# Performance work log

Measured on AMD Instinct MI355X. Metric: run time of the kernel, lower is better.

Reference implementation:

```python
import jax, jax.numpy as jnp
import numpy as np

ATTN_SCALE = 0.12
HEAD_DIM = 128


def _rms_norm(x):
    # F.rms_norm with no weight; eps defaults to machine eps of dtype
    eps = jnp.asarray(jnp.finfo(x.dtype).eps, x.dtype)
    return x * jax.lax.rsqrt(jnp.mean(x * x, axis=-1, keepdims=True) + eps)


def _rope(x):
    # x: [B, T, H, D]; standard rotary over (first-half, second-half) pairs
    T, D = x.shape[1], x.shape[-1]
    half = D // 2
    inv_freq = 1.0 / (10000.0 ** (jnp.arange(half, dtype=jnp.float32) / half))
    ang = jnp.arange(T, dtype=jnp.float32)[:, None] * inv_freq[None, :]  # [T, half]
    cos = jnp.cos(ang)[None, :, None, :].astype(x.dtype)
    sin = jnp.sin(ang)[None, :, None, :].astype(x.dtype)
    x1, x2 = x[..., :half], x[..., half:]
    return jnp.concatenate([x1 * cos - x2 * sin, x1 * sin + x2 * cos], axis=-1)


def setup_inputs() -> dict:
    key = jax.random.key(0)
    ks = jax.random.split(key, 4)
    B, T, dim, H, hd = 4, 2048, 1024, 8, HEAD_DIM
    hdim = H * hd
    std = 0.5 * dim ** (-0.5)
    bound = (3.0 ** 0.5) * std
    return {
        "x": jax.random.normal(ks[0], (B, T, dim), jnp.float32),
        "ve": jax.random.normal(ks[1], (B, T, hdim), jnp.float32),
        "qkv_w": jax.random.uniform(ks[2], (3, hdim, dim), jnp.float32, -bound, bound),
        "lambdas": jnp.array([0.5, 0.5], jnp.float32),
        "c_proj_w": jax.random.normal(ks[3], (dim, hdim), jnp.float32) * (hdim ** -0.5),
        "c_proj_b": jnp.zeros((dim,), jnp.float32),
    }


def reference(x, ve, qkv_w, lambdas, c_proj_w, c_proj_b):
    B, T, dim = x.shape
    hdim = qkv_w.shape[1]
    hd = HEAD_DIM
    H = hdim // hd
    # fused QKV projection: [B,T,3,H,hd]
    qkv = jnp.einsum('btd,ehd->bteh', x, qkv_w.reshape(3 * hdim, dim).reshape(3 * H, hd, dim).reshape(3 * hdim // hd, hd, dim))
    qkv = jnp.einsum('btd,fd->btf', x, qkv_w.reshape(3 * hdim, dim)).reshape(B, T, 3, H, hd)
    q, k, v = qkv[:, :, 0], qkv[:, :, 1], qkv[:, :, 2]  # each [B,T,H,hd]
    q, k = _rms_norm(q), _rms_norm(k)
    q, k = _rope(q), _rope(k)
    v = lambdas[0] * v + lambdas[1] * ve.reshape(B, T, H, hd)
    # causal SDPA with custom scale
    scores = jnp.einsum('bthd,bshd->bhts', q, k) * ATTN_SCALE  # [B,H,T,T]
    causal = jnp.tril(jnp.ones((T, T), dtype=bool))
    scores = jnp.where(causal[None, None], scores, jnp.finfo(scores.dtype).min)
    p = jax.nn.softmax(scores, axis=-1)
    y = jnp.einsum('bhts,bshd->bthd', p, v).reshape(B, T, hdim)
    return y @ c_proj_w.T + c_proj_b
```

## Files before the change

### kernel.cpp

```cpp
#include <hip/hip_runtime.h>
#include <math.h>

typedef unsigned short u16;
typedef short bf16x8 __attribute__((ext_vector_type(8)));
typedef u16 u16x2 __attribute__((ext_vector_type(2)));
typedef u16 u16x4 __attribute__((ext_vector_type(4)));
typedef u16 u16x8 __attribute__((ext_vector_type(8)));
typedef float f32x2 __attribute__((ext_vector_type(2)));
typedef float f32x4 __attribute__((ext_vector_type(4)));
typedef float f32x16 __attribute__((ext_vector_type(16)));

typedef __attribute__((address_space(1))) const void gvoid_t;
typedef __attribute__((address_space(3))) void lvoid_t;

__device__ __forceinline__ u16 f2bf(float f) {
  union { float f; unsigned u; } v; v.f = f;
  unsigned r = v.u + 0x7fffu + ((v.u >> 16) & 1u);
  return (u16)(r >> 16);
}
__device__ __forceinline__ float bf2f(u16 h) {
  union { unsigned u; float f; } v; v.u = ((unsigned)h) << 16;
  return v.f;
}
__device__ __forceinline__ f32x4 mfma16(bf16x8 a, bf16x8 b, f32x4 c) {
  return __builtin_amdgcn_mfma_f32_16x16x32_bf16(a, b, c, 0, 0, 0);
}
__device__ __forceinline__ f32x16 mfma32(bf16x8 a, bf16x8 b, f32x16 c) {
  return __builtin_amdgcn_mfma_f32_32x32x16_bf16(a, b, c, 0, 0, 0);
}
__device__ __forceinline__ void gload_lds16(const void* g, void* l) {
  __builtin_amdgcn_global_load_lds((gvoid_t*)g, (lvoid_t*)l, 16, 0, 0);
}
__device__ __forceinline__ unsigned cvtpk_bf16(float lo, float hi) {
  unsigned r;
  asm("v_cvt_pk_bf16_f32 %0, %1, %2" : "=v"(r) : "v"(lo), "v"(hi));
  return r;
}
__device__ __forceinline__ void pswap32(unsigned& a, unsigned& b) {
  asm("v_permlane32_swap_b32 %0, %1" : "+v"(a), "+v"(b));
}

#if __has_builtin(__builtin_amdgcn_exp2f)
#define EXPW(x) __builtin_amdgcn_exp2f(x)
#define SCALE_W 0.17312354f
#define DEFER_THR 11.5415603f
#else
#define EXPW(x) __expf(x)
#define SCALE_W 0.12f
#define DEFER_THR 8.0f
#endif

#define BAR() __builtin_amdgcn_s_barrier()
#define WAITLGKM()                          \
  asm volatile("s_waitcnt lgkmcnt(0)");     \
  __builtin_amdgcn_sched_barrier(0)
#define WAITVMC(N)                                    \
  do {                                                \
    __builtin_amdgcn_s_waitcnt(0x0F70 | (N));         \
    __builtin_amdgcn_sched_barrier(0);                \
  } while (0)

__global__ __launch_bounds__(256) void cvt_bf16_kernel(const float* __restrict__ in,
                                                       u16* __restrict__ out, int n4) {
  int i = blockIdx.x * 256 + threadIdx.x;
  if (i >= n4) return;
  f32x4 v = *(const f32x4*)(in + (size_t)i * 4);
  u16x4 o;
  o[0] = f2bf(v[0]); o[1] = f2bf(v[1]); o[2] = f2bf(v[2]); o[3] = f2bf(v[3]);
  *(u16x4*)(out + (size_t)i * 4) = o;
}

__global__ __launch_bounds__(256) void rope_tab_kernel(float* __restrict__ ct,
                                                       float* __restrict__ st) {
  int i = blockIdx.x * 256 + threadIdx.x;
  int t = i >> 6, j = i & 63;
  float inv = powf(10000.f, -(float)j * (1.0f / 64.0f));
  float ang = (float)t * inv;
  ct[i] = cosf(ang);
  st[i] = sinf(ang);
}

template <int BM, int OUTF32>
__global__ __launch_bounds__(512, 1) void gemm8p_kernel(
    const u16* __restrict__ A, const u16* __restrict__ B, void* __restrict__ C,
    const float* __restrict__ bias, int M, int N, int K, int nbn) {
  constexpr int AH = BM / 2;
  constexpr int WR = AH / 2;
  constexpr int MI = WR / 16;
  constexpr int NACC = 2 * MI;
  constexpr int AROUNDS = AH / 64;
  constexpr int SA = AROUNDS;
  constexpr int SB = 2;
  __shared__ u16 Alds[2][BM * 64];
  __shared__ u16 Blds[2][256 * 64];
  int nwg = gridDim.x;
  int cpx = nwg >> 3;
  int bid = blockIdx.x;
  int swz = (bid & 7) * cpx + (bid >> 3);
  int bm = swz / nbn, bn = swz % nbn;
  size_t m0 = (size_t)bm * BM, n0 = (size_t)bn * 256;
  int tid = threadIdx.x, wid = tid >> 6, lane = tid & 63;
  int wr = wid >> 2, wc = wid & 3, l15 = lane & 15, l4 = lane >> 4;
  int srow = tid >> 3, sch = tid & 7;

  const u16* Abase = A + m0 * K;
  const u16* Bbase = B + n0 * K;

  f32x4 acc[NACC][4];
#pragma unroll
  for (int m = 0; m < NACC; m++)
#pragma unroll
    for (int n = 0; n < 4; n++) acc[m][n] = f32x4{0.f, 0.f, 0.f, 0.f};

  auto stageA = [&](int buf, int kt, int half) {
#pragma unroll
    for (int r = 0; r < AROUNDS; ++r) {
      int row = AH * half + 64 * r + srow;
      gload_lds16(Abase + (size_t)row * K + kt * 64 + 8 * (sch ^ (row & 7)),
                  &Alds[buf][(AH * half + 64 * r + 8 * wid) * 64]);
    }
  };
  auto stageB = [&](int buf, int kt, int half) {
#pragma unroll
    for (int r = 0; r < 2; ++r) {
      int row = 128 * half + 64 * r + srow;
      gload_lds16(Bbase + (size_t)row * K + kt * 64 + 8 * (sch ^ (row & 7)),
                  &Blds[buf][(128 * half + 64 * r + 8 * wid) * 64]);
    }
  };
  auto rdA = [&](int buf, int half, bf16x8 (&a)[MI][2]) {
#pragma unroll
    for (int mi = 0; mi < MI; ++mi)
#pragma unroll
      for (int kk = 0; kk < 2; ++kk) {
        int row = AH * half + WR * wr + 16 * mi + l15;
        a[mi][kk] = *(const bf16x8*)((const char*)(&Alds[buf][0]) + row * 128 +
                                     ((kk * 64 + 16 * l4) ^ ((row & 7) << 4)));
      }
  };
  auto rdB = [&](int buf, int half, bf16x8 (&bb)[2][2]) {
#pragma unroll
    for (int ni = 0; ni < 2; ++ni)
#pragma unroll
      for (int kk = 0; kk < 2; ++kk) {
        int row = 64 * wc + 32 * half + 16 * ni + l15;
        bb[ni][kk] = *(const bf16x8*)((const char*)(&Blds[buf][0]) + row * 128 +
                                      ((kk * 64 + 16 * l4) ^ ((row & 7) << 4)));
      }
  };

#define QUAD(AF, BF, MH, NH)                                              \
  do {                                                                    \
    __builtin_amdgcn_s_setprio(1);                                        \
    _Pragma("unroll") for (int mi = 0; mi < MI; ++mi)                     \
        _Pragma("unroll") for (int ni = 0; ni < 2; ++ni)                  \
            _Pragma("unroll") for (int kk = 0; kk < 2; ++kk)              \
                acc[MI * MH + mi][2 * NH + ni] =                          \
        mfma16(AF[mi][kk], BF[ni][kk], acc[MI * MH + mi][2 * NH + ni]);   \
    __builtin_amdgcn_s_setprio(0);                                        \
  } while (0)

  stageB(0, 0, 0);
  stageA(0, 0, 0);
  stageB(0, 0, 1);
  stageA(0, 0, 1);
  WAITVMC(SA + SB);
  BAR();

  int nk = K >> 6;
  bf16x8 a0[MI][2], a1[MI][2], b0[2][2], b1[2][2];
  for (int t = 0; t < nk; ++t) {
    int buf = t & 1, nxt = buf ^ 1;
    bool pf = (t + 1 < nk);
    rdA(buf, 0, a0);
    rdB(buf, 0, b0);
    if (pf) { stageB(nxt, t + 1, 0); stageA(nxt, t + 1, 0); }
    BAR();
    WAITLGKM();
    QUAD(a0, b0, 0, 0);
    if (pf) { WAITVMC(2 * SA + SB); } else { WAITVMC(SA); }
    BAR();
    rdB(buf, 1, b1);
    if (pf) stageB(nxt, t + 1, 1);
    BAR();
    WAITLGKM();
    QUAD(a0, b1, 0, 1);
    if (pf) { WAITVMC(2 * SB + SA); } else { WAITVMC(0); }
    BAR();
    rdA(buf, 1, a1);
    if (pf) stageA(nxt, t + 1, 1);
    BAR();
    WAITLGKM();
    QUAD(a1, b0, 1, 0);
    BAR();
    QUAD(a1, b1, 1, 1);
    if (pf) WAITVMC(SA + SB);
    BAR();
  }

#pragma unroll
  for (int mi = 0; mi < NACC; ++mi) {
#pragma unroll
    for (int ni = 0; ni < 4; ++ni) {
      size_t row = m0 + AH * (mi / MI) + WR * wr + 16 * (mi % MI) + 4 * l4;
      size_t col = n0 + 64 * wc + 16 * ni + l15;
#pragma unroll
      for (int i = 0; i < 4; ++i) {
        float v = acc[mi][ni][i];
        if constexpr (OUTF32) {
          ((float*)C)[(row + i) * N + col] = v + bias[col];
        } else {
          ((u16*)C)[(row + i) * N + col] = f2bf(v);
        }
      }
    }
  }
#undef QUAD
}

__global__ __launch_bounds__(256) void transform_kernel(
    const u16* __restrict__ qkv, const float* __restrict__ ve,
    const float* __restrict__ lam, const float* __restrict__ ct,
    const float* __restrict__ st, u16* __restrict__ qn, u16* __restrict__ kn,
    u16* __restrict__ vt) {
  constexpr int T = 2048;
  __shared__ u16 vtile[64][136];
  int tt = blockIdx.x, bh = blockIdx.y;
  int b = bh >> 3, h = bh & 7;
  int tid = threadIdx.x, wid = tid >> 6, lane = tid & 63;
  int lsub = lane & 15, lrow = lane >> 4;
  float l0 = lam[0], l1 = lam[1];
  int d0 = 8 * lsub;
  float sgn = (lsub < 8) ? -1.f : 1.f;
  int jj = d0 & 63;
#pragma unroll
  for (int it = 0; it < 4; ++it) {
    int tl = wid * 16 + it * 4 + lrow;
    int t = tt * 64 + tl;
    size_t base = ((size_t)(b * T + t)) * 3072 + h * 128 + d0;
    u16x8 qraw = *(const u16x8*)(qkv + base);
    u16x8 kraw = *(const u16x8*)(qkv + base + 1024);
    u16x8 vraw = *(const u16x8*)(qkv + base + 2048);
    const float* vep = ve + ((size_t)(b * T + t)) * 1024 + h * 128 + d0;
    f32x4 ve0 = *(const f32x4*)(vep);
    f32x4 ve1 = *(const f32x4*)(vep + 4);
    float q[8], k[8];
    float sq = 0.f, sk = 0.f;
#pragma unroll
    for (int i = 0; i < 8; ++i) {
      q[i] = bf2f(qraw[i]); k[i] = bf2f(kraw[i]);
      sq += q[i] * q[i]; sk += k[i] * k[i];
    }
#pragma unroll
    for (int m = 1; m < 16; m <<= 1) {
      sq += __shfl_xor(sq, m);
      sk += __shfl_xor(sk, m);
    }
    float qs = rsqrtf(sq * (1.f / 128.f) + 1.1920929e-7f);
    float ks = rsqrtf(sk * (1.f / 128.f) + 1.1920929e-7f);
#pragma unroll
    for (int i = 0; i < 8; ++i) { q[i] *= qs; k[i] *= ks; }
    f32x4 c0 = *(const f32x4*)(ct + t * 64 + jj);
    f32x4 c1 = *(const f32x4*)(ct + t * 64 + jj + 4);
    f32x4 s0 = *(const f32x4*)(st + t * 64 + jj);
    f32x4 s1 = *(const f32x4*)(st + t * 64 + jj + 4);
    u16x8 oq, ok, ov;
#pragma unroll
    for (int i = 0; i < 8; ++i) {
      float qp = __shfl_xor(q[i], 8), kp = __shfl_xor(k[i], 8);
      float cc = (i < 4) ? c0[i & 3] : c1[i & 3];
      float ss = (i < 4) ? s0[i & 3] : s1[i & 3];
      oq[i] = f2bf(q[i] * cc + sgn * qp * ss);
      ok[i] = f2bf(k[i] * cc + sgn * kp * ss);
      float vv = (i < 4) ? ve0[i & 3] : ve1[i & 3];
      ov[i] = f2bf(l0 * bf2f(vraw[i]) + l1 * vv);
    }
    size_t orow = ((size_t)bh * T + t) * 128 + d0;
    *(u16x8*)(qn + orow) = oq;
    *(u16x8*)(kn + orow) = ok;
    *(u16x8*)&vtile[tl][d0] = ov;
  }
  __syncthreads();
#pragma unroll
  for (int it = 0; it < 4; ++it) {
    int ci = it * 256 + tid;
    int d = ci >> 3, c8 = ci & 7;
    u16x8 o;
#pragma unroll
    for (int u = 0; u < 8; u++) o[u] = vtile[c8 * 8 + u][d];
    *(u16x8*)(vt + ((size_t)bh * 128 + d) * T + tt * 64 + c8 * 8) = o;
  }
}

__global__ __launch_bounds__(256, 2) void attn_kernel(
    const u16* __restrict__ Qn, const u16* __restrict__ Kn,
    const u16* __restrict__ Vt, u16* __restrict__ Y) {
  constexpr int T = 2048;
  __shared__ u16 Klds[2][64 * 128];
  __shared__ u16 Vlds[2][128 * 64];
  int bid = blockIdx.x;
  int g = bid >> 5;
  int s = (g < 8) ? (15 - g) : (g - 8);
  int bh = bid & 31;
  int b = bh >> 3, h = bh & 7;
  int tid = threadIdx.x, wid = tid >> 6, lane = tid & 63;
  int l31 = lane & 31, hh = lane >> 5;
  const u16* Qb = Qn + (size_t)bh * T * 128;
  const u16* Kb = Kn + (size_t)bh * T * 128;
  const u16* Vb = Vt + (size_t)bh * 128 * T;
  int q0w = s * 128 + wid * 32;
  int qmaxw = q0w + 31;
  int ktend = 2 * s + 2;
  int qg = q0w + l31;

  bf16x8 qf[8];
  {
    const u16* qr = Qb + (size_t)(q0w + l31) * 128 + 8 * hh;
#pragma unroll
    for (int ks = 0; ks < 8; ks++) qf[ks] = *(const bf16x8*)(qr + 16 * ks);
  }
  f32x16 acc[4];
#pragma unroll
  for (int mt = 0; mt < 4; mt++)
#pragma unroll
    for (int r = 0; r < 16; r++) acc[mt][r] = 0.f;
  float m_run = -1e30f, l_run = 0.f;

  auto stage = [&](int buf, int kt) {
#pragma unroll
    for (int it = 0; it < 4; ++it) {
      int id = wid * 256 + it * 64 + lane;
      int r = id >> 4, c = id & 15;
      gload_lds16(Kb + (size_t)(kt * 64 + r) * 128 + 8 * (c ^ (r & 7)),
                  &Klds[buf][(size_t)(wid * 256 + it * 64) * 8]);
      int rv = id >> 3, cv = id & 7;
      gload_lds16(Vb + (size_t)rv * T + kt * 64 + 8 * (cv ^ (rv & 7)),
                  &Vlds[buf][(size_t)(wid * 256 + it * 64) * 8]);
    }
  };

  stage(0, 0);
  __syncthreads();

  for (int kt = 0; kt < ktend; ++kt) {
    int cur = kt & 1;
    if (kt + 1 < ktend) stage(cur ^ 1, kt + 1);
    if (kt * 64 <= qmaxw) {
      const char* kb = (const char*)&Klds[cur][0];
      const char* vb = (const char*)&Vlds[cur][0];
      int rswz = (l31 & 7) << 4;
      f32x16 st0, st1;
#pragma unroll
      for (int r = 0; r < 16; r++) { st0[r] = 0.f; st1[r] = 0.f; }
      __builtin_amdgcn_s_setprio(1);
#pragma unroll
      for (int ks = 0; ks < 8; ks++) {
        bf16x8 kf0 = *(const bf16x8*)(kb + ((l31 * 256 + 32 * ks + 16 * hh) ^ rswz));
        bf16x8 kf1 = *(const bf16x8*)(kb + (((32 + l31) * 256 + 32 * ks + 16 * hh) ^ rswz));
        st0 = mfma32(kf0, qf[ks], st0);
        st1 = mfma32(kf1, qf[ks], st1);
      }
      __builtin_amdgcn_s_setprio(0);
      bool edge = (kt == (qmaxw >> 6));
      if (edge) {
#pragma unroll
        for (int r = 0; r < 16; r++) {
          int kvb = kt * 64 + (r & 3) + 8 * (r >> 2) + 4 * hh;
          if (kvb > qg) st0[r] = -1e30f;
          if (kvb + 32 > qg) st1[r] = -1e30f;
        }
      }
      float m8[8];
#pragma unroll
      for (int r = 0; r < 8; r++)
        m8[r] = fmaxf(fmaxf(st0[r], st0[r + 8]), fmaxf(st1[r], st1[r + 8]));
#pragma unroll
      for (int r = 0; r < 4; r++) m8[r] = fmaxf(m8[r], m8[r + 4]);
      float pm = fmaxf(fmaxf(m8[0], m8[1]), fmaxf(m8[2], m8[3]));
      pm = fmaxf(pm, __shfl_xor(pm, 32));
      float pmn = pm * SCALE_W;
      bool nos = __all(pmn <= m_run + DEFER_THR);
      float mnew = nos ? m_run : fmaxf(m_run, pmn);
      if (!nos) {
        float alpha = EXPW(m_run - mnew);
        l_run *= alpha;
#pragma unroll
        for (int mt = 0; mt < 4; mt++)
#pragma unroll
          for (int r = 0; r < 16; r++) acc[mt][r] *= alpha;
        m_run = mnew;
      }
      float sa = 0.f, sb = 0.f, sc = 0.f, sd = 0.f;
#pragma unroll
      for (int r = 0; r < 4; r++) {
        st0[r]      = EXPW(fmaf(st0[r],      SCALE_W, -mnew)); sa += st0[r];
        st0[r + 4]  = EXPW(fmaf(st0[r + 4],  SCALE_W, -mnew)); sb += st0[r + 4];
        st0[r + 8]  = EXPW(fmaf(st0[r + 8],  SCALE_W, -mnew)); sc += st0[r + 8];
        st0[r + 12] = EXPW(fmaf(st0[r + 12], SCALE_W, -mnew)); sd += st0[r + 12];
        st1[r]      = EXPW(fmaf(st1[r],      SCALE_W, -mnew)); sa += st1[r];
        st1[r + 4]  = EXPW(fmaf(st1[r + 4],  SCALE_W, -mnew)); sb += st1[r + 4];
        st1[r + 8]  = EXPW(fmaf(st1[r + 8],  SCALE_W, -mnew)); sc += st1[r + 8];
        st1[r + 12] = EXPW(fmaf(st1[r + 12], SCALE_W, -mnew)); sd += st1[r + 12];
      }
      float ps = (sa + sb) + (sc + sd);
      ps += __shfl_xor(ps, 32);
      l_run += ps;
      unsigned pA0[4], pB0[4], pA1[4], pB1[4];
#pragma unroll
      for (int rr = 0; rr < 4; rr++) {
        pA0[rr] = cvtpk_bf16(st0[4 * rr], st0[4 * rr + 1]);
        pB0[rr] = cvtpk_bf16(st0[4 * rr + 2], st0[4 * rr + 3]);
        pA1[rr] = cvtpk_bf16(st1[4 * rr], st1[4 * rr + 1]);
        pB1[rr] = cvtpk_bf16(st1[4 * rr + 2], st1[4 * rr + 3]);
      }
      bf16x8 pf[4];
#pragma unroll
      for (int ks2 = 0; ks2 < 4; ks2++) {
        int k1 = ks2 & 1;
        unsigned a0, b0, a1, b1;
        if (ks2 < 2) { a0 = pA0[2 * k1]; b0 = pA0[2 * k1 + 1]; a1 = pB0[2 * k1]; b1 = pB0[2 * k1 + 1]; }
        else         { a0 = pA1[2 * k1]; b0 = pA1[2 * k1 + 1]; a1 = pB1[2 * k1]; b1 = pB1[2 * k1 + 1]; }
        pswap32(a0, b0);
        pswap32(a1, b1);
        union { unsigned w[4]; bf16x8 v; } u;
        u.w[0] = a0; u.w[1] = a1; u.w[2] = b0; u.w[3] = b1;
        pf[ks2] = u.v;
      }
      __builtin_amdgcn_s_setprio(1);
#pragma unroll
      for (int mt = 0; mt < 4; mt++) {
        int row = 32 * mt + l31;
#pragma unroll
        for (int ks2 = 0; ks2 < 4; ks2++) {
          bf16x8 vf = *(const bf16x8*)(vb + ((row * 128 + 32 * ks2 + 16 * hh) ^ rswz));
          acc[mt] = mfma32(vf, pf[ks2], acc[mt]);
        }
      }
      __builtin_amdgcn_s_setprio(0);
    }
    __syncthreads();
  }
  float linv = 1.f / l_run;
  size_t yrow = (size_t)b * T + q0w + l31;
  u16* yp = Y + yrow * 1024 + h * 128;
#pragma unroll
  for (int mt = 0; mt < 4; mt++) {
#pragma unroll
    for (int rr = 0; rr < 4; rr++) {
      u16x4 o;
#pragma unroll
      for (int i = 0; i < 4; i++) o[i] = f2bf(acc[mt][4 * rr + i] * linv);
      *(u16x4*)(yp + 32 * mt + 8 * rr + 4 * hh) = o;
    }
  }
}

extern "C" void kernel_launch(void* const* d_in, const int* in_sizes, int n_in,
                              void* d_out, int out_size, void* d_ws, size_t ws_size,
                              hipStream_t stream) {
  (void)in_sizes; (void)n_in; (void)out_size; (void)ws_size;
  const float* x = (const float*)d_in[0];
  const float* ve = (const float*)d_in[1];
  const float* qkvw = (const float*)d_in[2];
  const float* lam = (const float*)d_in[3];
  const float* cpw = (const float*)d_in[4];
  const float* cpb = (const float*)d_in[5];
  float* out = (float*)d_out;
  char* ws = (char*)d_ws;

  u16* xb   = (u16*)(ws + 0);
  u16* wqkv = (u16*)(ws + 16777216);
  u16* wp   = (u16*)(ws + 23068672);
  u16* qkv  = (u16*)(ws + 25165824);
  u16* qn   = (u16*)(ws + 75497472);
  u16* kn   = (u16*)(ws + 92274688);
  u16* vt   = (u16*)(ws + 109051904);
  float* ctab = (float*)(ws + 125829120);
  float* stab = (float*)(ws + 126353408);
  u16* y = xb;

  rope_tab_kernel<<<512, 256, 0, stream>>>(ctab, stab);
  cvt_bf16_kernel<<<8192, 256, 0, stream>>>(x, xb, 2097152);
  cvt_bf16_kernel<<<3072, 256, 0, stream>>>(qkvw, wqkv, 786432);
  cvt_bf16_kernel<<<1024, 256, 0, stream>>>(cpw, wp, 262144);
  gemm8p_kernel<256, 0><<<384, 512, 0, stream>>>(xb, wqkv, qkv, nullptr, 8192, 3072, 1024, 12);
  transform_kernel<<<dim3(32, 32), 256, 0, stream>>>(qkv, ve, lam, ctab, stab, qn, kn, vt);
  attn_kernel<<<512, 256, 0, stream>>>(qn, kn, vt, y);
  gemm8p_kernel<128, 1><<<256, 512, 0, stream>>>(y, wp, out, cpb, 8192, 1024, 1024, 4);
}
```

Baseline: 203.5 us.

## Restructure GEMM into two-phase pipeline, regroup tile swizzle, explicit attn prefetch waits

The GEMM main loop drops from four barrier-separated phases to two. Both B halves are loaded and issued together, and s_setprio is hoisted around pairs of MFMA quads. The block-to-tile mapping now groups four M tiles per N column for better L2 reuse. The attention loop replaces __syncthreads with an explicit vmcnt wait plus barrier, so the next tile's loads overlap with the wait on the current tile. Fewer barriers should cut stalls, but the B fragments stay live longer and the new wait counts must be correct.

```diff
diff --git a/kernel.cpp b/kernel.cpp
--- a/kernel.cpp
+++ b/kernel.cpp
@@ -81,7 +81,7 @@
 }
 
 template <int BM, int OUTF32>
-__global__ __launch_bounds__(512, 1) void gemm8p_kernel(
+__global__ __launch_bounds__(512, 1) void gemm2ph_kernel(
     const u16* __restrict__ A, const u16* __restrict__ B, void* __restrict__ C,
     const float* __restrict__ bias, int M, int N, int K, int nbn) {
   constexpr int AH = BM / 2;
@@ -97,7 +97,8 @@
   int cpx = nwg >> 3;
   int bid = blockIdx.x;
   int swz = (bid & 7) * cpx + (bid >> 3);
-  int bm = swz / nbn, bn = swz % nbn;
+  int bm = (swz & 3) + 4 * (swz / (4 * nbn));
+  int bn = (swz >> 2) % nbn;
   size_t m0 = (size_t)bm * BM, n0 = (size_t)bn * 256;
   int tid = threadIdx.x, wid = tid >> 6, lane = tid & 63;
   int wr = wid >> 2, wc = wid & 3, l15 = lane & 15, l4 = lane >> 4;
@@ -151,20 +152,18 @@
 
 #define QUAD(AF, BF, MH, NH)                                              \
   do {                                                                    \
-    __builtin_amdgcn_s_setprio(1);                                        \
     _Pragma("unroll") for (int mi = 0; mi < MI; ++mi)                     \
         _Pragma("unroll") for (int ni = 0; ni < 2; ++ni)                  \
             _Pragma("unroll") for (int kk = 0; kk < 2; ++kk)              \
                 acc[MI * MH + mi][2 * NH + ni] =                          \
         mfma16(AF[mi][kk], BF[ni][kk], acc[MI * MH + mi][2 * NH + ni]);   \
-    __builtin_amdgcn_s_setprio(0);                                        \
   } while (0)
 
   stageB(0, 0, 0);
+  stageB(0, 0, 1);
   stageA(0, 0, 0);
-  stageB(0, 0, 1);
   stageA(0, 0, 1);
-  WAITVMC(SA + SB);
+  WAITVMC(SA);
   BAR();
 
   int nk = K >> 6;
@@ -174,27 +173,25 @@
     bool pf = (t + 1 < nk);
     rdA(buf, 0, a0);
     rdB(buf, 0, b0);
-    if (pf) { stageB(nxt, t + 1, 0); stageA(nxt, t + 1, 0); }
+    rdB(buf, 1, b1);
+    if (pf) { stageB(nxt, t + 1, 0); stageB(nxt, t + 1, 1); stageA(nxt, t + 1, 0); }
     BAR();
     WAITLGKM();
+    __builtin_amdgcn_s_setprio(1);
     QUAD(a0, b0, 0, 0);
-    if (pf) { WAITVMC(2 * SA + SB); } else { WAITVMC(SA); }
-    BAR();
-    rdB(buf, 1, b1);
-    if (pf) stageB(nxt, t + 1, 1);
-    BAR();
-    WAITLGKM();
     QUAD(a0, b1, 0, 1);
+    __builtin_amdgcn_s_setprio(0);
     if (pf) { WAITVMC(2 * SB + SA); } else { WAITVMC(0); }
     BAR();
     rdA(buf, 1, a1);
     if (pf) stageA(nxt, t + 1, 1);
     BAR();
     WAITLGKM();
+    __builtin_amdgcn_s_setprio(1);
     QUAD(a1, b0, 1, 0);
-    BAR();
     QUAD(a1, b1, 1, 1);
-    if (pf) WAITVMC(SA + SB);
+    __builtin_amdgcn_s_setprio(0);
+    if (pf) { WAITVMC(SA); } else { WAITVMC(0); }
     BAR();
   }
 
@@ -340,11 +337,16 @@
   };
 
   stage(0, 0);
-  __syncthreads();
 
   for (int kt = 0; kt < ktend; ++kt) {
     int cur = kt & 1;
-    if (kt + 1 < ktend) stage(cur ^ 1, kt + 1);
+    if (kt + 1 < ktend) {
+      stage(cur ^ 1, kt + 1);
+      WAITVMC(8);
+    } else {
+      WAITVMC(0);
+    }
+    BAR();
     if (kt * 64 <= qmaxw) {
       const char* kb = (const char*)&Klds[cur][0];
       const char* vb = (const char*)&Vlds[cur][0];
@@ -438,7 +440,7 @@
       }
       __builtin_amdgcn_s_setprio(0);
     }
-    __syncthreads();
+    BAR();
   }
   float linv = 1.f / l_run;
   size_t yrow = (size_t)b * T + q0w + l31;
@@ -483,8 +485,8 @@
   cvt_bf16_kernel<<<8192, 256, 0, stream>>>(x, xb, 2097152);
   cvt_bf16_kernel<<<3072, 256, 0, stream>>>(qkvw, wqkv, 786432);
   cvt_bf16_kernel<<<1024, 256, 0, stream>>>(cpw, wp, 262144);
-  gemm8p_kernel<256, 0><<<384, 512, 0, stream>>>(xb, wqkv, qkv, nullptr, 8192, 3072, 1024, 12);
+  gemm2ph_kernel<256, 0><<<384, 512, 0, stream>>>(xb, wqkv, qkv, nullptr, 8192, 3072, 1024, 12);
   transform_kernel<<<dim3(32, 32), 256, 0, stream>>>(qkv, ve, lam, ctab, stab, qn, kn, vt);
   attn_kernel<<<512, 256, 0, stream>>>(qn, kn, vt, y);
-  gemm8p_kernel<128, 1><<<256, 512, 0, stream>>>(y, wp, out, cpb, 8192, 1024, 1024, 4);
-}
+  gemm2ph_kernel<128, 1><<<256, 512, 0, stream>>>(y, wp, out, cpb, 8192, 1024, 1024, 4);
+}
```

New measurement: 202.2 us. No clear change (-0.7%).
